# Kernel optimization log

Measured on AMD Instinct MI355X. Metric: run time of the kernel, lower is better.

Reference implementation:

```python
import jax, jax.numpy as jnp
import numpy as np

B, S, H = 8, 1024, 1536          # batch, seq, hidden_size
NH, HD, AH = 8, 96, 768          # heads after head_ratio=2, head_size=hidden/16, all_head_size
K = 7                            # conv_kernel_size
IM = 3072                        # intermediate_size
EPS = 1e-12                      # ConvBert layer_norm_eps


def _ln(x, g, b):
    m = x.mean(-1, keepdims=True)
    v = ((x - m) ** 2).mean(-1, keepdims=True)
    return (x - m) / jnp.sqrt(v + EPS) * g + b


def _windows(x, k):
    # x: [B,S,C] -> sliding windows [B,S,k,C] with 'same' padding ((k-1)//2 each side, k odd)
    p = (k - 1) // 2
    xp = jnp.pad(x, ((0, 0), (p, p), (0, 0)))
    idx = jnp.arange(x.shape[1])[:, None] + jnp.arange(k)[None, :]
    return xp[:, idx, :]


def _forward(embed, wq, bq, wk, bk, wv, bv, dw, pw, sep_b, wck, bck, wco, bco,
             wso, bso, ln1_g, ln1_b, wi, bi, wo, bo, ln2_g, ln2_b, wd, bd):
    b, s, _ = embed.shape
    # --- projections (weights stored [in,out]) ---
    q = embed @ wq + bq            # [B,S,AH]
    kk = embed @ wk + bk
    v = embed @ wv + bv
    # --- SeparableConv1D on hidden states: depthwise(k=7) then pointwise + bias ---
    win_h = _windows(embed, K)                             # [B,S,K,H]
    dconv = jnp.einsum('bskc,ck->bsc', win_h, dw)          # depthwise, [B,S,H]
    sep = dconv @ pw + sep_b                               # pointwise, [B,S,AH]
    # --- span dynamic conv kernels ---
    conv_attn = sep * q                                    # [B,S,AH]
    ck = (conv_attn @ wck + bck).reshape(b, s, NH, K)      # [B,S,NH,K]
    ck = jax.nn.softmax(ck, axis=-1)
    co = embed @ wco + bco                                 # [B,S,AH]
    win_co = _windows(co, K).reshape(b, s, K, NH, HD)      # [B,S,K,NH,HD]
    conv_out = jnp.einsum('bskhd,bshk->bshd', win_co, ck)  # [B,S,NH,HD]
    # --- standard self-attention on the reduced heads ---
    qh = q.reshape(b, s, NH, HD)
    kh = kk.reshape(b, s, NH, HD)
    vh = v.reshape(b, s, NH, HD)
    scores = jnp.einsum('bqhd,bkhd->bhqk', qh, kh) / jnp.sqrt(jnp.float32(HD))
    probs = jax.nn.softmax(scores, axis=-1)
    ctx = jnp.einsum('bhqk,bkhd->bqhd', probs, vh)         # [B,S,NH,HD]
    # --- concat attention heads with conv heads -> [B,S,2*NH,HD] -> [B,S,H] ---
    ctx = jnp.concatenate([ctx, conv_out], axis=2).reshape(b, s, H)
    # --- self output (dropout is identity at inference) ---
    attn_out = _ln(ctx @ wso + bso + embed, ln1_g, ln1_b)
    # --- FFN ---
    inter = jax.nn.gelu(attn_out @ wi + bi, approximate=False)
    layer_out = _ln(inter @ wo + bo + attn_out, ln2_g, ln2_b)
    # --- global max pooling over sequence + linear decoder ---
    pooled = layer_out.max(axis=1)                         # [B,H]
    logits = pooled @ wd + bd                              # [B,1]
    return logits


def setup_inputs() -> dict:
    key = jax.random.key(0)
    ks = jax.random.split(key, 32)
    rn = lambda i, shape, s=0.02: jax.random.normal(ks[i], shape, jnp.float32) * s
    d = {}
    d['embed'] = jax.random.normal(ks[0], (B, S, H), jnp.float32)
    d['wq'] = rn(1, (H, AH)); d['bq'] = jnp.zeros((AH,), jnp.float32)
    d['wk'] = rn(2, (H, AH)); d['bk'] = jnp.zeros((AH,), jnp.float32)
    d['wv'] = rn(3, (H, AH)); d['bv'] = jnp.zeros((AH,), jnp.float32)
    d['dw'] = rn(4, (H, K)); d['pw'] = rn(5, (H, AH)); d['sep_b'] = jnp.zeros((AH,), jnp.float32)
    d['wck'] = rn(6, (AH, NH * K)); d['bck'] = jnp.zeros((NH * K,), jnp.float32)
    d['wco'] = rn(7, (H, AH)); d['bco'] = jnp.zeros((AH,), jnp.float32)
    d['wso'] = rn(8, (H, H)); d['bso'] = jnp.zeros((H,), jnp.float32)
    d['ln1_g'] = jnp.ones((H,), jnp.float32); d['ln1_b'] = jnp.zeros((H,), jnp.float32)
    d['wi'] = rn(9, (H, IM)); d['bi'] = jnp.zeros((IM,), jnp.float32)
    d['wo'] = rn(10, (IM, H)); d['bo'] = jnp.zeros((H,), jnp.float32)
    d['ln2_g'] = jnp.ones((H,), jnp.float32); d['ln2_b'] = jnp.zeros((H,), jnp.float32)
    d['wd'] = jax.random.uniform(ks[11], (H, 1), jnp.float32, -0.1, 0.1)
    d['bd'] = jnp.zeros((1,), jnp.float32)
    return d


def reference(embed, wq, bq, wk, bk, wv, bv, dw, pw, sep_b, wck, bck, wco, bco,
              wso, bso, ln1_g, ln1_b, wi, bi, wo, bo, ln2_g, ln2_b, wd, bd):
    return _forward(embed, wq, bq, wk, bk, wv, bv, dw, pw, sep_b, wck, bck, wco, bco,
                    wso, bso, ln1_g, ln1_b, wi, bi, wo, bo, ln2_g, ln2_b, wd, bd)
```

## Files before the change

kernel.cpp:

```cpp
#include <hip/hip_runtime.h>


typedef __bf16 bf16_t;
typedef short s16x8 __attribute__((ext_vector_type(8)));
typedef float f32x4 __attribute__((ext_vector_type(4)));

#define BB  8
#define SS  1024
#define HH  1536
#define NHH 8
#define HDD 96
#define AHH 768
#define IMM 3072

__device__ __forceinline__ float rd_adapt(const void* p, long long i, int isbf) {
    return isbf ? (float)((const bf16_t*)p)[i] : ((const float*)p)[i];
}

__device__ __forceinline__ float gelu_f(float v) {
    float u = v * (0.7978845608f + 0.0356774081f * v * v);
    float e = __expf(2.0f * u);
    float t = 1.0f - 2.0f / (e + 1.0f);
    return 0.5f * v * (1.0f + t);
}

__device__ __forceinline__ void gl2lds16(const bf16_t* g, bf16_t* l) {
    __builtin_amdgcn_global_load_lds(
        (__attribute__((address_space(1))) const void*)g,
        (__attribute__((address_space(3))) void*)l, 16, 0, 0);
}

#define FENCE() asm volatile("" ::: "memory")
#define BARRIER() do { FENCE(); __builtin_amdgcn_s_barrier(); FENCE(); } while (0)

__global__ __launch_bounds__(256)
void detect_kernel(const void* __restrict__ embed, int* __restrict__ flag)
{
    __shared__ int cnt[256];
    int t = threadIdx.x;
    float x = (float)((const bf16_t*)embed)[t];
    float a = fabsf(x);
    cnt[t] = (a > 1e-3f && a < 50.0f) ? 1 : 0;
    __syncthreads();
    for (int o = 128; o > 0; o >>= 1) { if (t < o) cnt[t] += cnt[t + o]; __syncthreads(); }
    if (t == 0) *flag = (cnt[0] >= 205) ? 1 : 0;
}

__global__ __launch_bounds__(256)
void convert_embed(const void* __restrict__ in, bf16_t* __restrict__ out,
                   const int* __restrict__ flagp)
{
    int isbf = *flagp;
    long long i0 = ((long long)blockIdx.x * 256 + threadIdx.x) * 8;
    if (isbf) {
        *(s16x8*)(out + i0) = *(const s16x8*)((const bf16_t*)in + i0);
    } else {
        const float* f = (const float*)in;
        #pragma unroll
        for (int j = 0; j < 8; j++) out[i0 + j] = (bf16_t)f[i0 + j];
    }
}

__global__ __launch_bounds__(256)
void concat_bias(const void* __restrict__ b0, const void* __restrict__ b1,
                 const void* __restrict__ b2, const void* __restrict__ b3,
                 bf16_t* __restrict__ out, const int* __restrict__ flagp)
{
    int isbf = *flagp;
    int t = blockIdx.x * 256 + threadIdx.x;
    int sel = t / 768, off = t - sel * 768;
    const void* src = (sel == 0) ? b0 : (sel == 1) ? b1 : (sel == 2) ? b2 : b3;
    out[t] = (bf16_t)rd_adapt(src, off, isbf);
}

__global__ __launch_bounds__(512, 2)
void gemm256(const bf16_t* __restrict__ A, const bf16_t* __restrict__ Bt,
             bf16_t* __restrict__ C, const void* __restrict__ bias,
             const bf16_t* __restrict__ emul, int lde, const int* __restrict__ flagp,
             int M, int N, int Kd, int lda, int ldb, int ldc, int act, int tilesN)
{
    __shared__ bf16_t Sm[65536];
    char* smb = (char*)Sm;
    int isbf = flagp ? *flagp : 1;

    int nwg = gridDim.x;
    int orig = blockIdx.x;
    int q = nwg >> 3, r = nwg & 7;
    int xcd = orig & 7, lid = orig >> 3;
    int wg = (xcd < r ? xcd * (q + 1) : r * (q + 1) + (xcd - r) * q) + lid;
    int row0 = (wg / tilesN) * 256;
    int col0 = (wg % tilesN) * 256;

    int tid = threadIdx.x;
    int wave = tid >> 6, lane = tid & 63;
    int wm = wave >> 2, wn = wave & 3;
    int lm = lane & 15, kq = lane >> 4;

    int srow = lane >> 3;
    int scol = 8 * ((lane & 7) ^ srow);

    auto stageA2 = [&](int kt, int h, int bufo) {
        #pragma unroll
        for (int l = 0; l < 2; l++) {
            int rloc = h * 128 + (2 * wave + l) * 8 + srow;
            gl2lds16(A + (long long)(row0 + rloc) * lda + kt * 64 + scol,
                     (bf16_t*)(smb + bufo * 32768 + h * 16384 + (2 * wave + l) * 1024));
        }
    };
    auto stageB2 = [&](int kt, int h, int bufo) {
        #pragma unroll
        for (int l = 0; l < 2; l++) {
            int rloc = h * 128 + (2 * wave + l) * 8 + srow;
            gl2lds16(Bt + (long long)(col0 + rloc) * ldb + kt * 64 + scol,
                     (bf16_t*)(smb + 65536 + bufo * 32768 + h * 16384 + (2 * wave + l) * 1024));
        }
    };

    int xo = (lm & 7) << 4;
    int cofs[2];
    cofs[0] = (kq * 16) ^ xo;
    cofs[1] = (64 + kq * 16) ^ xo;
    int aoffs[8];
    #pragma unroll
    for (int ip = 0; ip < 8; ip++) aoffs[ip] = (wm * 128 + ip * 16 + lm) * 128;
    int boffs[4];
    #pragma unroll
    for (int j = 0; j < 4; j++) boffs[j] = 65536 + (wn * 64 + j * 16 + lm) * 128;

    f32x4 acc[8][4] = {};
    s16x8 af[4][2], bf0[2][2], bf1[2][2];

    int KT = Kd >> 6;

    stageA2(0, 0, 0);
    stageB2(0, 0, 0);
    stageA2(0, 1, 0);
    stageB2(0, 1, 0);
    int k1 = min(1, KT - 1);
    stageB2(k1, 0, 1);
    stageA2(k1, 0, 1);
    asm volatile("s_waitcnt vmcnt(4)" ::: "memory");
    BARRIER();

    for (int t = 0; t < KT; t++) {
        int buf = t & 1;
        int bA = buf * 32768;
        int ob = buf ^ 1;
        int tn1 = min(t + 1, KT - 1), tn2 = min(t + 2, KT - 1);

        #pragma unroll
        for (int i = 0; i < 4; i++)
            #pragma unroll
            for (int s = 0; s < 2; s++)
                af[i][s] = *(const s16x8*)(smb + bA + aoffs[i] + cofs[s]);
        #pragma unroll
        for (int j = 0; j < 2; j++)
            #pragma unroll
            for (int s = 0; s < 2; s++)
                bf0[j][s] = *(const s16x8*)(smb + bA + boffs[j] + cofs[s]);
        stageA2(tn1, 1, ob);
        BARRIER();
        asm volatile("s_waitcnt lgkmcnt(0)" ::: "memory");
        __builtin_amdgcn_sched_barrier(0);
        __builtin_amdgcn_s_setprio(1);
        #pragma unroll
        for (int i = 0; i < 4; i++)
            #pragma unroll
            for (int j = 0; j < 2; j++) {
                acc[i][j] = __builtin_amdgcn_mfma_f32_16x16x32_bf16(af[i][0], bf0[j][0], acc[i][j], 0, 0, 0);
                acc[i][j] = __builtin_amdgcn_mfma_f32_16x16x32_bf16(af[i][1], bf0[j][1], acc[i][j], 0, 0, 0);
            }
        __builtin_amdgcn_s_setprio(0);
        BARRIER();

        #pragma unroll
        for (int j = 0; j < 2; j++)
            #pragma unroll
            for (int s = 0; s < 2; s++)
                bf1[j][s] = *(const s16x8*)(smb + bA + boffs[2 + j] + cofs[s]);
        stageB2(tn1, 1, ob);
        BARRIER();
        asm volatile("s_waitcnt lgkmcnt(0)" ::: "memory");
        __builtin_amdgcn_sched_barrier(0);
        __builtin_amdgcn_s_setprio(1);
        #pragma unroll
        for (int i = 0; i < 4; i++)
            #pragma unroll
            for (int j = 0; j < 2; j++) {
                acc[i][2 + j] = __builtin_amdgcn_mfma_f32_16x16x32_bf16(af[i][0], bf1[j][0], acc[i][2 + j], 0, 0, 0);
                acc[i][2 + j] = __builtin_amdgcn_mfma_f32_16x16x32_bf16(af[i][1], bf1[j][1], acc[i][2 + j], 0, 0, 0);
            }
        __builtin_amdgcn_s_setprio(0);
        BARRIER();

        #pragma unroll
        for (int i = 0; i < 4; i++)
            #pragma unroll
            for (int s = 0; s < 2; s++)
                af[i][s] = *(const s16x8*)(smb + bA + aoffs[4 + i] + cofs[s]);
        stageB2(tn2, 0, buf);
        BARRIER();
        asm volatile("s_waitcnt lgkmcnt(0)" ::: "memory");
        __builtin_amdgcn_sched_barrier(0);
        __builtin_amdgcn_s_setprio(1);
        #pragma unroll
        for (int i = 0; i < 4; i++)
            #pragma unroll
            for (int j = 0; j < 2; j++) {
                acc[4 + i][2 + j] = __builtin_amdgcn_mfma_f32_16x16x32_bf16(af[i][0], bf1[j][0], acc[4 + i][2 + j], 0, 0, 0);
                acc[4 + i][2 + j] = __builtin_amdgcn_mfma_f32_16x16x32_bf16(af[i][1], bf1[j][1], acc[4 + i][2 + j], 0, 0, 0);
            }
        __builtin_amdgcn_s_setprio(0);
        BARRIER();

        stageA2(tn2, 0, buf);
        BARRIER();
        __builtin_amdgcn_s_setprio(1);
        #pragma unroll
        for (int i = 0; i < 4; i++)
            #pragma unroll
            for (int j = 0; j < 2; j++) {
                acc[4 + i][j] = __builtin_amdgcn_mfma_f32_16x16x32_bf16(af[i][0], bf0[j][0], acc[4 + i][j], 0, 0, 0);
                acc[4 + i][j] = __builtin_amdgcn_mfma_f32_16x16x32_bf16(af[i][1], bf0[j][1], acc[4 + i][j], 0, 0, 0);
            }
        __builtin_amdgcn_s_setprio(0);
        asm volatile("s_waitcnt vmcnt(4)" ::: "memory");
        BARRIER();
    }

    #pragma unroll
    for (int j = 0; j < 4; j++) {
        int gcol = col0 + wn * 64 + j * 16 + lm;
        float bv = bias ? rd_adapt(bias, gcol, isbf) : 0.0f;
        #pragma unroll
        for (int ip = 0; ip < 8; ip++) {
            int grow0 = row0 + wm * 128 + ip * 16 + kq * 4;
            #pragma unroll
            for (int r = 0; r < 4; r++) {
                float v = acc[ip][j][r] + bv;
                if (emul) v *= (float)emul[(long long)(grow0 + r) * lde + gcol];
                if (act) v = gelu_f(v);
                C[(long long)(grow0 + r) * ldc + gcol] = (bf16_t)v;
            }
        }
    }
}

__global__ __launch_bounds__(256)
void gemm_tile(const bf16_t* __restrict__ A, const bf16_t* __restrict__ Bt,
               bf16_t* __restrict__ C, const void* __restrict__ bias, long long biasOff,
               const bf16_t* __restrict__ emul, int lde, const int* __restrict__ flagp,
               int M, int N, int Kd, int lda, int ldb, int ldc,
               float scale, int act, int beta, int nlim)
{
    __shared__ bf16_t Sm[16384];

    int isbf = flagp ? *flagp : 1;
    int tid  = threadIdx.x;
    int wave = tid >> 6, lane = tid & 63;
    int wm = wave >> 1, wn = wave & 1;
    int row0 = blockIdx.x * 128;
    int col0 = blockIdx.y * 128;
    int lm = lane & 15;
    int kq = lane >> 4;

    int sr = tid >> 2;
    int sc = (tid & 3) * 8;
    const bf16_t* ga0 = A + (long long)(row0 + sr) * lda + sc;
    const bf16_t* ga1 = A + (long long)(row0 + 64 + sr) * lda + sc;
    int br0 = min(col0 + sr, nlim);
    int br1 = min(col0 + 64 + sr, nlim);
    const bf16_t* gb0 = Bt + (long long)br0 * ldb + sc;
    const bf16_t* gb1 = Bt + (long long)br1 * ldb + sc;
    bf16_t* lw = Sm + wave * 512;

    f32x4 acc[4][4] = {};

    for (int k0 = 0; k0 < Kd; k0 += 64) {
        #pragma unroll
        for (int h = 0; h < 2; h++) {
            int kh = k0 + h * 32;
            gl2lds16(ga0 + kh, lw + h * 4096);
            gl2lds16(ga1 + kh, lw + h * 4096 + 2048);
            gl2lds16(gb0 + kh, lw + 8192 + h * 4096);
            gl2lds16(gb1 + kh, lw + 8192 + h * 4096 + 2048);
        }
        __syncthreads();

        s16x8 af[2][4], bfr[2][4];
        #pragma unroll
        for (int h = 0; h < 2; h++) {
            #pragma unroll
            for (int i = 0; i < 4; i++)
                af[h][i] = *(const s16x8*)(Sm + h * 4096 + (wm * 64 + i * 16 + lm) * 32 + kq * 8);
            #pragma unroll
            for (int j = 0; j < 4; j++)
                bfr[h][j] = *(const s16x8*)(Sm + 8192 + h * 4096 + (wn * 64 + j * 16 + lm) * 32 + kq * 8);
        }
        #pragma unroll
        for (int i = 0; i < 4; i++)
            #pragma unroll
            for (int j = 0; j < 4; j++) {
                acc[i][j] = __builtin_amdgcn_mfma_f32_16x16x32_bf16(af[0][i], bfr[0][j], acc[i][j], 0, 0, 0);
                acc[i][j] = __builtin_amdgcn_mfma_f32_16x16x32_bf16(af[1][i], bfr[1][j], acc[i][j], 0, 0, 0);
            }
        __syncthreads();
    }

    #pragma unroll
    for (int j = 0; j < 4; j++) {
        int gcol = col0 + wn * 64 + j * 16 + lm;
        if (gcol >= N) continue;
        float bv = bias ? rd_adapt(bias, biasOff + gcol, isbf) : 0.0f;
        #pragma unroll
        for (int i = 0; i < 4; i++) {
            int grow0 = row0 + wm * 64 + i * 16 + kq * 4;
            #pragma unroll
            for (int r = 0; r < 4; r++) {
                float v = acc[i][j][r] * scale + bv;
                long long ci = (long long)(grow0 + r) * ldc + gcol;
                if (beta) v += (float)C[ci];
                if (emul) v *= (float)emul[(long long)(grow0 + r) * lde + gcol];
                if (act) v = gelu_f(v);
                C[ci] = (bf16_t)v;
            }
        }
    }
}

__global__ __launch_bounds__(256, 2)
void flash_attn(const bf16_t* __restrict__ qkv, const bf16_t* __restrict__ vT,
                bf16_t* __restrict__ ctxcat)
{
    const float ascale = 0.1020620726159658f;
    __shared__ bf16_t Pl[4 * 32 * 136];

    int bh = blockIdx.x;
    int b = bh >> 3, h = bh & 7;
    const bf16_t* Qp = qkv  + (long long)b * SS * 3072 + h * HDD;
    const bf16_t* Kp = qkv  + (long long)b * SS * 3072 + 768 + h * HDD;
    const bf16_t* Vt = vT   + (long long)b * AHH * SS + (long long)h * HDD * SS;
    bf16_t*       Op = ctxcat + (long long)b * SS * HH + h * HDD;

    int tid = threadIdx.x, wave = tid >> 6, lane = tid & 63;
    int lm = lane & 15, kq = lane >> 4;
    int q0 = blockIdx.y * 128 + wave * 32;
    bf16_t* Pw = Pl + wave * 32 * 136;

    s16x8 aq[2][3];
    #pragma unroll
    for (int i = 0; i < 2; i++)
        #pragma unroll
        for (int kf = 0; kf < 3; kf++)
            aq[i][kf] = *(const s16x8*)(Qp + (long long)(q0 + i * 16 + lm) * 3072 + kf * 32 + kq * 8);

    f32x4 Oacc[2][6] = {};
    float mrow[2][4], lrow[2][4];
    #pragma unroll
    for (int i = 0; i < 2; i++)
        #pragma unroll
        for (int r = 0; r < 4; r++) { mrow[i][r] = -1e30f; lrow[i][r] = 0.0f; }

    for (int kt = 0; kt < 8; kt++) {
        f32x4 S[2][8] = {};
        #pragma unroll
        for (int j = 0; j < 8; j++) {
            s16x8 bk[3];
            #pragma unroll
            for (int kf = 0; kf < 3; kf++)
                bk[kf] = *(const s16x8*)(Kp + (long long)(kt * 128 + j * 16 + lm) * 3072 + kf * 32 + kq * 8);
            #pragma unroll
            for (int i = 0; i < 2; i++)
                #pragma unroll
                for (int kf = 0; kf < 3; kf++)
                    S[i][j] = __builtin_amdgcn_mfma_f32_16x16x32_bf16(aq[i][kf], bk[kf], S[i][j], 0, 0, 0);
        }

        float mnew[2][4];
        #pragma unroll
        for (int i = 0; i < 2; i++) {
            #pragma unroll
            for (int r = 0; r < 4; r++) {
                float mx = -1e30f;
                #pragma unroll
                for (int j = 0; j < 8; j++) mx = fmaxf(mx, S[i][j][r]);
                #pragma unroll
                for (int msk = 1; msk <= 8; msk <<= 1) mx = fmaxf(mx, __shfl_xor(mx, msk));
                mnew[i][r] = fmaxf(mrow[i][r], mx * ascale);
            }
        }
        #pragma unroll
        for (int i = 0; i < 2; i++) {
            #pragma unroll
            for (int r = 0; r < 4; r++) {
                float al = __expf(mrow[i][r] - mnew[i][r]);
                lrow[i][r] *= al;
                #pragma unroll
                for (int n = 0; n < 6; n++) Oacc[i][n][r] *= al;
                mrow[i][r] = mnew[i][r];
            }
        }
        float psum[2][4] = {};
        __syncthreads();
        #pragma unroll
        for (int i = 0; i < 2; i++) {
            #pragma unroll
            for (int j = 0; j < 8; j++) {
                #pragma unroll
                for (int r = 0; r < 4; r++) {
                    float p = __expf(S[i][j][r] * ascale - mnew[i][r]);
                    psum[i][r] += p;
                    Pw[(i * 16 + kq * 4 + r) * 136 + j * 16 + lm] = (bf16_t)p;
                }
            }
        }
        #pragma unroll
        for (int i = 0; i < 2; i++) {
            #pragma unroll
            for (int r = 0; r < 4; r++) {
                float t = psum[i][r];
                #pragma unroll
                for (int msk = 1; msk <= 8; msk <<= 1) t += __shfl_xor(t, msk);
                lrow[i][r] += t;
            }
        }
        __syncthreads();

        s16x8 ap[2][4];
        #pragma unroll
        for (int i = 0; i < 2; i++)
            #pragma unroll
            for (int kf = 0; kf < 4; kf++)
                ap[i][kf] = *(const s16x8*)(Pw + (i * 16 + lm) * 136 + kf * 32 + kq * 8);
        #pragma unroll
        for (int n = 0; n < 6; n++) {
            s16x8 bv[4];
            #pragma unroll
            for (int kf = 0; kf < 4; kf++)
                bv[kf] = *(const s16x8*)(Vt + (long long)(n * 16 + lm) * SS + kt * 128 + kf * 32 + kq * 8);
            #pragma unroll
            for (int i = 0; i < 2; i++)
                #pragma unroll
                for (int kf = 0; kf < 4; kf++)
                    Oacc[i][n] = __builtin_amdgcn_mfma_f32_16x16x32_bf16(ap[i][kf], bv[kf], Oacc[i][n], 0, 0, 0);
        }
    }

    #pragma unroll
    for (int i = 0; i < 2; i++) {
        #pragma unroll
        for (int n = 0; n < 6; n++) {
            #pragma unroll
            for (int r = 0; r < 4; r++) {
                int row = q0 + i * 16 + kq * 4 + r;
                int col = n * 16 + lm;
                Op[(long long)row * HH + col] = (bf16_t)(Oacc[i][n][r] / lrow[i][r]);
            }
        }
    }
}

__global__ __launch_bounds__(256)
void transpose_pad(const void* __restrict__ in, bf16_t* __restrict__ out,
                   int R, int C, int ldin, long long inOff,
                   long long sInB, long long sOutB, const int* __restrict__ flagp)
{
    __shared__ bf16_t t[32][33];
    int isbf = flagp ? *flagp : 1;
    int z = blockIdx.z;
    long long base = inOff + (long long)z * sInB;
    bf16_t* op = out + (long long)z * sOutB;
    int tx = threadIdx.x & 31, ty = threadIdx.x >> 5;
    int cb = blockIdx.x * 32, rb = blockIdx.y * 32;
    #pragma unroll
    for (int rr = ty; rr < 32; rr += 8) {
        int r = rb + rr, c = cb + tx;
        t[rr][tx] = (c < C) ? (bf16_t)rd_adapt(in, base + (long long)r * ldin + c, isbf)
                            : (bf16_t)0.0f;
    }
    __syncthreads();
    #pragma unroll
    for (int rr = ty; rr < 32; rr += 8) {
        int c = cb + rr;
        op[(long long)c * R + rb + tx] = t[tx][rr];
    }
}

__global__ __launch_bounds__(256)
void dconv_kernel(const bf16_t* __restrict__ ebuf, const void* __restrict__ dw,
                  bf16_t* __restrict__ out, const int* __restrict__ flagp)
{
    int isbf = *flagp;
    long long i = (long long)blockIdx.x * 256 + threadIdx.x;
    int c = (int)(i % HH);
    long long bs = i / HH;
    int s = (int)(bs % SS);
    float acc = 0.0f;
    #pragma unroll
    for (int k = 0; k < 7; k++) {
        int ss = s + k - 3;
        if (ss >= 0 && ss < SS)
            acc += (float)ebuf[(bs + (k - 3)) * HH + c] * rd_adapt(dw, c * 7 + k, isbf);
    }
    out[i] = (bf16_t)acc;
}

__global__ __launch_bounds__(256)
void ck_softmax(const bf16_t* __restrict__ ck, float* __restrict__ ckp)
{
    int i = blockIdx.x * 256 + threadIdx.x;
    if (i >= BB * SS * NHH) return;
    int h = i % NHH;
    long long bs = i / NHH;
    const bf16_t* src = ck + bs * 64 + h * 7;
    float v[7], mx = -1e30f;
    #pragma unroll
    for (int k = 0; k < 7; k++) { v[k] = (float)src[k]; mx = fmaxf(mx, v[k]); }
    float sum = 0.0f;
    #pragma unroll
    for (int k = 0; k < 7; k++) { v[k] = expf(v[k] - mx); sum += v[k]; }
    float inv = 1.0f / sum;
    float* dst = ckp + bs * 56 + h * 7;
    #pragma unroll
    for (int k = 0; k < 7; k++) dst[k] = v[k] * inv;
}

__global__ __launch_bounds__(256)
void conv_out_kernel(const bf16_t* __restrict__ co, int ldco,
                     const float* __restrict__ ckp, bf16_t* __restrict__ ctxcat)
{
    long long i = (long long)blockIdx.x * 256 + threadIdx.x;
    int hd = (int)(i % AHH);
    long long bs = i / AHH;
    int s = (int)(bs % SS);
    int h = hd / HDD;
    const float* w = ckp + bs * 56 + h * 7;
    float acc = 0.0f;
    #pragma unroll
    for (int k = 0; k < 7; k++) {
        int ss = s + k - 3;
        if (ss >= 0 && ss < SS)
            acc += (float)co[(bs + (k - 3)) * ldco + hd] * w[k];
    }
    ctxcat[bs * HH + AHH + hd] = (bf16_t)acc;
}

__global__ __launch_bounds__(256)
void ln_kernel(const bf16_t* __restrict__ y, const bf16_t* __restrict__ res,
               const void* __restrict__ g, const void* __restrict__ bta,
               bf16_t* __restrict__ outb, const int* __restrict__ flagp)
{
    int isbf = *flagp;
    long long row = blockIdx.x;
    const bf16_t* yp = y + row * HH;
    const bf16_t* rp = res + row * HH;
    int tid = threadIdx.x;
    float x[6], s = 0.0f, s2 = 0.0f;
    #pragma unroll
    for (int i = 0; i < 6; i++) {
        int c = tid + i * 256;
        float v = (float)yp[c] + (float)rp[c];
        x[i] = v; s += v; s2 += v * v;
    }
    __shared__ float sa[256], sb[256];
    sa[tid] = s; sb[tid] = s2; __syncthreads();
    for (int o = 128; o > 0; o >>= 1) {
        if (tid < o) { sa[tid] += sa[tid + o]; sb[tid] += sb[tid + o]; }
        __syncthreads();
    }
    float mean = sa[0] * (1.0f / HH);
    float var  = sb[0] * (1.0f / HH) - mean * mean;
    float inv  = rsqrtf(var + 1e-12f);
    #pragma unroll
    for (int i = 0; i < 6; i++) {
        int c = tid + i * 256;
        float v = (x[i] - mean) * inv * rd_adapt(g, c, isbf) + rd_adapt(bta, c, isbf);
        outb[row * HH + c] = (bf16_t)v;
    }
}

__global__ __launch_bounds__(256)
void maxpool_p1(const bf16_t* __restrict__ lo, float* __restrict__ part)
{
    int sc = blockIdx.x, b = blockIdx.y;
    int tid = threadIdx.x;
    const bf16_t* p = lo + ((long long)b * SS + sc * 32) * HH;
    float m[6];
    #pragma unroll
    for (int k = 0; k < 6; k++) m[k] = -1e30f;
    for (int r = 0; r < 32; r++)
        #pragma unroll
        for (int k = 0; k < 6; k++)
            m[k] = fmaxf(m[k], (float)p[(long long)r * HH + k * 256 + tid]);
    #pragma unroll
    for (int k = 0; k < 6; k++)
        part[((long long)b * 32 + sc) * HH + k * 256 + tid] = m[k];
}

__global__ __launch_bounds__(256)
void maxpool_p2(const float* __restrict__ part, float* __restrict__ pooled)
{
    int i = blockIdx.x * 256 + threadIdx.x;
    if (i >= BB * HH) return;
    int b = i / HH, c = i % HH;
    float m = -1e30f;
    for (int ch = 0; ch < 32; ch++) m = fmaxf(m, part[((long long)b * 32 + ch) * HH + c]);
    pooled[i] = m;
}

__global__ __launch_bounds__(256)
void decoder_kernel(const float* __restrict__ pooled, const void* __restrict__ wd,
                    const void* __restrict__ bd, void* __restrict__ out,
                    const int* __restrict__ flagp)
{
    int isbf = *flagp;
    int b = blockIdx.x;
    int tid = threadIdx.x;
    float s = 0.0f;
    #pragma unroll
    for (int i = 0; i < 6; i++) {
        int c = tid + i * 256;
        s += pooled[b * HH + c] * rd_adapt(wd, c, isbf);
    }
    __shared__ float sa[256];
    sa[tid] = s; __syncthreads();
    for (int o = 128; o > 0; o >>= 1) { if (tid < o) sa[tid] += sa[tid + o]; __syncthreads(); }
    if (tid == 0) {
        float r = sa[0] + rd_adapt(bd, 0, isbf);
        if (isbf) ((bf16_t*)out)[b] = (bf16_t)r;
        else      ((float*)out)[b]  = r;
    }
}

extern "C" void kernel_launch(void* const* d_in, const int* in_sizes, int n_in,
                              void* d_out, int out_size, void* d_ws, size_t ws_size,
                              hipStream_t stream)
{
    const void* embed = d_in[0];
    const void* wq  = d_in[1];  const void* bq  = d_in[2];
    const void* wk  = d_in[3];  const void* bk  = d_in[4];
    const void* wv  = d_in[5];  const void* bv  = d_in[6];
    const void* dw  = d_in[7];  const void* pw  = d_in[8];  const void* sep_b = d_in[9];
    const void* wck = d_in[10]; const void* bck = d_in[11];
    const void* wco = d_in[12]; const void* bco = d_in[13];
    const void* wso = d_in[14]; const void* bso = d_in[15];
    const void* ln1g = d_in[16]; const void* ln1b = d_in[17];
    const void* wi  = d_in[18]; const void* bi  = d_in[19];
    const void* wo  = d_in[20]; const void* bo  = d_in[21];
    const void* ln2g = d_in[22]; const void* ln2b = d_in[23];
    const void* wd  = d_in[24]; const void* bd  = d_in[25];
    (void)ws_size; (void)in_sizes; (void)n_in; (void)out_size;

    char* ws = (char*)d_ws;
    char* A  = ws;
    char* B  = ws + 50331648;
    char* C_ = ws + 75497472;
    char* D  = ws + 88080384;
    char* E  = ws + 113246208;
    char* F  = ws + 138412032;
    char* XP = ws + 143130624;

    bf16_t* qkvco  = (bf16_t*)A;
    bf16_t* ybuf   = (bf16_t*)A;
    bf16_t* interb = (bf16_t*)A;
    bf16_t* lout   = (bf16_t*)A;
    bf16_t* wT_all = (bf16_t*)B;
    bf16_t* dconvb = (bf16_t*)B;
    bf16_t* ckb    = (bf16_t*)B;
    float*  ckp    = (float*)(B + 1310720);
    bf16_t* vT     = (bf16_t*)B;
    bf16_t* wfT    = (bf16_t*)B;
    bf16_t* sepb   = (bf16_t*)C_;
    float*  mpart  = (float*)C_;
    bf16_t* ctxcat = (bf16_t*)D;
    bf16_t* attn   = (bf16_t*)D;
    bf16_t* ebuf   = (bf16_t*)E;
    bf16_t* y2     = (bf16_t*)E;
    bf16_t* wT     = (bf16_t*)F;
    int*    flag   = (int*)XP;
    float*  pooled = (float*)(XP + 256);
    bf16_t* cbias  = (bf16_t*)(XP + 256 + 49152);

    dim3 blk(256);

    auto gemm_big = [&](const bf16_t* Ai, const bf16_t* Bt, bf16_t* Ci, const void* bias,
                        const bf16_t* emul, int lde, const int* fl,
                        int M, int N, int Kd, int lda, int ldb, int ldc, int act) {
        int tn = N / 256;
        dim3 g((M / 256) * tn);
        gemm256<<<g, dim3(512), 0, stream>>>(Ai, Bt, Ci, bias, emul, lde, fl,
                                             M, N, Kd, lda, ldb, ldc, act, tn);
    };
    auto gemm = [&](const bf16_t* Ai, const bf16_t* Bt, bf16_t* Ci, const void* bias,
                    long long biasOff, const bf16_t* emul, int lde, const int* fl,
                    int M, int N, int Kd, int lda, int ldb, int ldc,
                    float scale, int act, int beta, int nlim) {
        dim3 g(M / 128, (N + 127) / 128, 1);
        gemm_tile<<<g, blk, 0, stream>>>(Ai, Bt, Ci, bias, biasOff, emul, lde, fl,
                                         M, N, Kd, lda, ldb, ldc,
                                         scale, act, beta, nlim);
    };
    auto transpose = [&](const void* in, bf16_t* out, int R, int Cc, int Cpad, int ldin,
                         long long inOff, int batch, long long sInB, long long sOutB,
                         const int* fl) {
        dim3 g(Cpad / 32, R / 32, batch);
        transpose_pad<<<g, blk, 0, stream>>>(in, out, R, Cc, ldin, inOff, sInB, sOutB, fl);
    };

    detect_kernel<<<dim3(1), blk, 0, stream>>>(embed, flag);
    convert_embed<<<dim3(6144), blk, 0, stream>>>(embed, ebuf, flag);

    transpose(wq,  wT_all + 0ll * 768 * 1536, 1536, 768, 768, 768, 0, 1, 0, 0, flag);
    transpose(wk,  wT_all + 1ll * 768 * 1536, 1536, 768, 768, 768, 0, 1, 0, 0, flag);
    transpose(wv,  wT_all + 2ll * 768 * 1536, 1536, 768, 768, 768, 0, 1, 0, 0, flag);
    transpose(wco, wT_all + 3ll * 768 * 1536, 1536, 768, 768, 768, 0, 1, 0, 0, flag);
    concat_bias<<<dim3(12), blk, 0, stream>>>(bq, bk, bv, bco, cbias, flag);
    gemm_big(ebuf, wT_all, qkvco, cbias, nullptr, 0, nullptr,
             8192, 3072, 1536, HH, HH, 3072, 0);

    dconv_kernel<<<dim3((BB * SS * HH) / 256), blk, 0, stream>>>(ebuf, dw, dconvb, flag);
    transpose(pw, wT, 1536, 768, 768, 768, 0, 1, 0, 0, flag);
    gemm_big(dconvb, wT, sepb, sep_b, qkvco, 3072, flag,
             8192, 768, 1536, HH, HH, AHH, 0);

    transpose(wck, wT, 768, 56, 128, 56, 0, 1, 0, 0, flag);
    gemm(sepb, wT, ckb, bck, 0, nullptr, 0, flag,
         8192, 56, 768, AHH, AHH, 64, 1.0f, 0, 0, 127);
    ck_softmax<<<dim3((BB * SS * NHH) / 256), blk, 0, stream>>>(ckb, ckp);
    conv_out_kernel<<<dim3((BB * SS * AHH) / 256), blk, 0, stream>>>(qkvco + 2304, 3072, ckp, ctxcat);

    transpose(qkvco, vT, 1024, 768, 768, 3072, 1536, 8, 1024ll * 3072, 768ll * 1024, nullptr);
    flash_attn<<<dim3(64, 8), blk, 0, stream>>>(qkvco, vT, ctxcat);

    transpose(wso, wT, 1536, 1536, 1536, 1536, 0, 1, 0, 0, flag);
    gemm_big(ctxcat, wT, ybuf, bso, nullptr, 0, flag,
             8192, 1536, 1536, HH, HH, HH, 0);
    ln_kernel<<<dim3(8192), blk, 0, stream>>>(ybuf, ebuf, ln1g, ln1b, attn, flag);

    transpose(wi, wfT, 1536, 3072, 3072, 3072, 0, 1, 0, 0, flag);
    gemm_big(attn, wfT, interb, bi, nullptr, 0, flag,
             8192, 3072, 1536, HH, HH, IMM, 1);
    transpose(wo, wfT, 3072, 1536, 1536, 1536, 0, 1, 0, 0, flag);
    gemm_big(interb, wfT, y2, bo, nullptr, 0, flag,
             8192, 1536, 3072, IMM, IMM, HH, 0);
    ln_kernel<<<dim3(8192), blk, 0, stream>>>(y2, attn, ln2g, ln2b, lout, flag);

    maxpool_p1<<<dim3(32, 8), blk, 0, stream>>>(lout, mpart);
    maxpool_p2<<<dim3(48), blk, 0, stream>>>(mpart, pooled);
    decoder_kernel<<<dim3(BB), blk, 0, stream>>>(pooled, wd, bd, d_out, flag);
}
```

Baseline: 944.4 us.

## Software-pipeline LDS fragment loads across MFMA phases in big GEMM, use small GEMM for pointwise

Restructures the main big-GEMM K loop so each phase loads the next phase's A/B fragments from LDS while the current MFMAs run. Partial lgkmcnt waits replace the full waits, and the next tile's first fragments are prefetched at the end of the iteration. This uses double fragment registers (af0/af1) to hide LDS latency behind MFMA work, at the cost of extra register pressure. Separately, the pointwise-conv GEMM (N=768) is switched from gemm_big to the generic gemm path, presumably for a better tile count or occupancy at that size.

```diff
diff --git a/kernel.cpp b/kernel.cpp
--- a/kernel.cpp
+++ b/kernel.cpp
@@ -128,38 +128,77 @@
     for (int j = 0; j < 4; j++) boffs[j] = 65536 + (wn * 64 + j * 16 + lm) * 128;
 
     f32x4 acc[8][4] = {};
-    s16x8 af[4][2], bf0[2][2], bf1[2][2];
+    s16x8 af0[4][2], af1[4][2], bf0[2][2], bf1[2][2];
 
     int KT = Kd >> 6;
 
     stageA2(0, 0, 0);
+    stageA2(0, 1, 0);
     stageB2(0, 0, 0);
-    stageA2(0, 1, 0);
     stageB2(0, 1, 0);
     int k1 = min(1, KT - 1);
     stageB2(k1, 0, 1);
     stageA2(k1, 0, 1);
     asm volatile("s_waitcnt vmcnt(4)" ::: "memory");
     BARRIER();
+    #pragma unroll
+    for (int i = 0; i < 4; i++)
+        #pragma unroll
+        for (int s = 0; s < 2; s++)
+            af0[i][s] = *(const s16x8*)(smb + aoffs[i] + cofs[s]);
+    #pragma unroll
+    for (int j = 0; j < 2; j++)
+        #pragma unroll
+        for (int s = 0; s < 2; s++)
+            bf0[j][s] = *(const s16x8*)(smb + boffs[j] + cofs[s]);
 
     for (int t = 0; t < KT; t++) {
         int buf = t & 1;
         int bA = buf * 32768;
         int ob = buf ^ 1;
+        int bN = ob * 32768;
         int tn1 = min(t + 1, KT - 1), tn2 = min(t + 2, KT - 1);
 
+        BARRIER();
+        #pragma unroll
+        for (int j = 0; j < 2; j++)
+            #pragma unroll
+            for (int s = 0; s < 2; s++)
+                bf1[j][s] = *(const s16x8*)(smb + bA + boffs[2 + j] + cofs[s]);
+        stageA2(tn1, 1, ob);
+        asm volatile("s_waitcnt lgkmcnt(4)" ::: "memory");
+        __builtin_amdgcn_sched_barrier(0);
+        __builtin_amdgcn_s_setprio(1);
         #pragma unroll
         for (int i = 0; i < 4; i++)
             #pragma unroll
+            for (int j = 0; j < 2; j++) {
+                acc[i][j] = __builtin_amdgcn_mfma_f32_16x16x32_bf16(af0[i][0], bf0[j][0], acc[i][j], 0, 0, 0);
+                acc[i][j] = __builtin_amdgcn_mfma_f32_16x16x32_bf16(af0[i][1], bf0[j][1], acc[i][j], 0, 0, 0);
+            }
+        __builtin_amdgcn_s_setprio(0);
+
+        BARRIER();
+        #pragma unroll
+        for (int i = 0; i < 4; i++)
+            #pragma unroll
             for (int s = 0; s < 2; s++)
-                af[i][s] = *(const s16x8*)(smb + bA + aoffs[i] + cofs[s]);
-        #pragma unroll
-        for (int j = 0; j < 2; j++)
-            #pragma unroll
-            for (int s = 0; s < 2; s++)
-                bf0[j][s] = *(const s16x8*)(smb + bA + boffs[j] + cofs[s]);
-        stageA2(tn1, 1, ob);
+                af1[i][s] = *(const s16x8*)(smb + bA + aoffs[4 + i] + cofs[s]);
+        stageB2(tn1, 1, ob);
+        asm volatile("s_waitcnt lgkmcnt(8)" ::: "memory");
+        __builtin_amdgcn_sched_barrier(0);
+        __builtin_amdgcn_s_setprio(1);
+        #pragma unroll
+        for (int i = 0; i < 4; i++)
+            #pragma unroll
+            for (int j = 0; j < 2; j++) {
+                acc[i][2 + j] = __builtin_amdgcn_mfma_f32_16x16x32_bf16(af0[i][0], bf1[j][0], acc[i][2 + j], 0, 0, 0);
+                acc[i][2 + j] = __builtin_amdgcn_mfma_f32_16x16x32_bf16(af0[i][1], bf1[j][1], acc[i][2 + j], 0, 0, 0);
+            }
+        __builtin_amdgcn_s_setprio(0);
+
         BARRIER();
+        stageB2(tn2, 0, buf);
         asm volatile("s_waitcnt lgkmcnt(0)" ::: "memory");
         __builtin_amdgcn_sched_barrier(0);
         __builtin_amdgcn_s_setprio(1);
@@ -167,65 +206,34 @@
         for (int i = 0; i < 4; i++)
             #pragma unroll
             for (int j = 0; j < 2; j++) {
-                acc[i][j] = __builtin_amdgcn_mfma_f32_16x16x32_bf16(af[i][0], bf0[j][0], acc[i][j], 0, 0, 0);
-                acc[i][j] = __builtin_amdgcn_mfma_f32_16x16x32_bf16(af[i][1], bf0[j][1], acc[i][j], 0, 0, 0);
+                acc[4 + i][2 + j] = __builtin_amdgcn_mfma_f32_16x16x32_bf16(af1[i][0], bf1[j][0], acc[4 + i][2 + j], 0, 0, 0);
+                acc[4 + i][2 + j] = __builtin_amdgcn_mfma_f32_16x16x32_bf16(af1[i][1], bf1[j][1], acc[4 + i][2 + j], 0, 0, 0);
             }
         __builtin_amdgcn_s_setprio(0);
+
         BARRIER();
-
-        #pragma unroll
-        for (int j = 0; j < 2; j++)
-            #pragma unroll
-            for (int s = 0; s < 2; s++)
-                bf1[j][s] = *(const s16x8*)(smb + bA + boffs[2 + j] + cofs[s]);
-        stageB2(tn1, 1, ob);
-        BARRIER();
-        asm volatile("s_waitcnt lgkmcnt(0)" ::: "memory");
-        __builtin_amdgcn_sched_barrier(0);
-        __builtin_amdgcn_s_setprio(1);
-        #pragma unroll
-        for (int i = 0; i < 4; i++)
-            #pragma unroll
-            for (int j = 0; j < 2; j++) {
-                acc[i][2 + j] = __builtin_amdgcn_mfma_f32_16x16x32_bf16(af[i][0], bf1[j][0], acc[i][2 + j], 0, 0, 0);
-                acc[i][2 + j] = __builtin_amdgcn_mfma_f32_16x16x32_bf16(af[i][1], bf1[j][1], acc[i][2 + j], 0, 0, 0);
-            }
-        __builtin_amdgcn_s_setprio(0);
-        BARRIER();
-
-        #pragma unroll
-        for (int i = 0; i < 4; i++)
-            #pragma unroll
-            for (int s = 0; s < 2; s++)
-                af[i][s] = *(const s16x8*)(smb + bA + aoffs[4 + i] + cofs[s]);
-        stageB2(tn2, 0, buf);
-        BARRIER();
-        asm volatile("s_waitcnt lgkmcnt(0)" ::: "memory");
-        __builtin_amdgcn_sched_barrier(0);
-        __builtin_amdgcn_s_setprio(1);
-        #pragma unroll
-        for (int i = 0; i < 4; i++)
-            #pragma unroll
-            for (int j = 0; j < 2; j++) {
-                acc[4 + i][2 + j] = __builtin_amdgcn_mfma_f32_16x16x32_bf16(af[i][0], bf1[j][0], acc[4 + i][2 + j], 0, 0, 0);
-                acc[4 + i][2 + j] = __builtin_amdgcn_mfma_f32_16x16x32_bf16(af[i][1], bf1[j][1], acc[4 + i][2 + j], 0, 0, 0);
-            }
-        __builtin_amdgcn_s_setprio(0);
-        BARRIER();
-
         stageA2(tn2, 0, buf);
-        BARRIER();
-        __builtin_amdgcn_s_setprio(1);
-        #pragma unroll
-        for (int i = 0; i < 4; i++)
-            #pragma unroll
-            for (int j = 0; j < 2; j++) {
-                acc[4 + i][j] = __builtin_amdgcn_mfma_f32_16x16x32_bf16(af[i][0], bf0[j][0], acc[4 + i][j], 0, 0, 0);
-                acc[4 + i][j] = __builtin_amdgcn_mfma_f32_16x16x32_bf16(af[i][1], bf0[j][1], acc[4 + i][j], 0, 0, 0);
-            }
-        __builtin_amdgcn_s_setprio(0);
         asm volatile("s_waitcnt vmcnt(4)" ::: "memory");
         BARRIER();
+        #pragma unroll
+        for (int i = 0; i < 4; i++)
+            #pragma unroll
+            for (int s = 0; s < 2; s++)
+                af0[i][s] = *(const s16x8*)(smb + bN + aoffs[i] + cofs[s]);
+        __builtin_amdgcn_s_setprio(1);
+        #pragma unroll
+        for (int i = 0; i < 4; i++)
+            #pragma unroll
+            for (int j = 0; j < 2; j++) {
+                acc[4 + i][j] = __builtin_amdgcn_mfma_f32_16x16x32_bf16(af1[i][0], bf0[j][0], acc[4 + i][j], 0, 0, 0);
+                acc[4 + i][j] = __builtin_amdgcn_mfma_f32_16x16x32_bf16(af1[i][1], bf0[j][1], acc[4 + i][j], 0, 0, 0);
+            }
+        __builtin_amdgcn_s_setprio(0);
+        #pragma unroll
+        for (int j = 0; j < 2; j++)
+            #pragma unroll
+            for (int s = 0; s < 2; s++)
+                bf0[j][s] = *(const s16x8*)(smb + bN + boffs[j] + cofs[s]);
     }
 
     #pragma unroll
@@ -720,8 +728,8 @@
 
     dconv_kernel<<<dim3((BB * SS * HH) / 256), blk, 0, stream>>>(ebuf, dw, dconvb, flag);
     transpose(pw, wT, 1536, 768, 768, 768, 0, 1, 0, 0, flag);
-    gemm_big(dconvb, wT, sepb, sep_b, qkvco, 3072, flag,
-             8192, 768, 1536, HH, HH, AHH, 0);
+    gemm(dconvb, wT, sepb, sep_b, 0, qkvco, 3072, flag,
+         8192, 768, 1536, HH, HH, AHH, 1.0f, 0, 0, 767);
 
     transpose(wck, wT, 768, 56, 128, 56, 0, 1, 0, 0, flag);
     gemm(sepb, wT, ckb, bck, 0, nullptr, 0, flag,
```

After: 890.3 us. -5.7%, faster.
